# Kernel tuning notes

Measured on AMD Instinct MI355X. Metric: run time of the kernel, lower is better.

The kernel has to match this reference:

```python
import math
import jax, jax.numpy as jnp
import numpy as np

B, T, C, H = 2, 2048, 1024, 16
D = C // H


def get_slopes(n):
    def pow2_slopes(n):
        start = 2.0 ** (-(2.0 ** (-(math.log2(n) - 3))))
        return [start * (start ** i) for i in range(n)]
    if math.log2(n).is_integer():
        return pow2_slopes(n)
    c = 2 ** math.floor(math.log2(n))
    return pow2_slopes(c) + get_slopes(2 * c)[0::2][: n - c]


def setup_inputs() -> dict:
    key = jax.random.key(0)
    ks = jax.random.split(key, 5)
    std = 0.02
    x = jax.random.normal(ks[0], (B, T, C), dtype=jnp.float32)
    Wq = std * jax.random.normal(ks[1], (C, C), dtype=jnp.float32)
    Wk = std * jax.random.normal(ks[2], (C, C), dtype=jnp.float32)
    Wv = std * jax.random.normal(ks[3], (C, C), dtype=jnp.float32)
    Wo = (std / math.sqrt(24)) * jax.random.normal(ks[4], (C, C), dtype=jnp.float32)
    z = jnp.zeros((C,), dtype=jnp.float32)
    return {"x": x, "Wq": Wq, "bq": z, "Wk": Wk, "bk": z, "Wv": Wv, "bv": z, "Wo": Wo, "bo": z}


def reference(x, Wq, bq, Wk, bk, Wv, bv, Wo, bo):
    b, t, c = x.shape
    h, d = H, c // H
    # qkv projections: nn.Linear computes x @ W.T + b
    q = (x @ Wq.T + bq).reshape(b, t, h, d).transpose(0, 2, 1, 3)  # [B,H,T,D]
    k = (x @ Wk.T + bk).reshape(b, t, h, d).transpose(0, 2, 1, 3)
    v = (x @ Wv.T + bv).reshape(b, t, h, d).transpose(0, 2, 1, 3)

    att = jnp.einsum("bhqd,bhkd->bhqk", q, k) * (1.0 / math.sqrt(d))

    # ALiBi bias: -slope_h * (i - j) on the lower triangle, 0 above
    slopes = jnp.asarray(get_slopes(h), dtype=x.dtype)  # [H]
    i = jnp.arange(t)
    rel = jnp.tril(i[:, None] - i[None, :]).astype(x.dtype)  # [T,T]
    alibi = -slopes[:, None, None] * rel  # [H,T,T]
    att = att + alibi[None, :, :, :]

    causal = jnp.tril(jnp.ones((t, t), dtype=bool))
    att = jnp.where(causal[None, None, :, :], att, -jnp.inf)
    att = jax.nn.softmax(att, axis=-1)

    y = jnp.einsum("bhqk,bhkd->bhqd", att, v)
    y = y.transpose(0, 2, 1, 3).reshape(b, t, c)
    return y @ Wo.T + bo
```

## Files before the change

kernel.cpp:

```cpp
#include <hip/hip_runtime.h>
#include <hip/hip_bf16.h>
#include <cstdint>
#include <cstddef>

#define B_ 2
#define T_ 2048
#define C_ 1024
#define H_ 16
#define D_ 64
#define BT_ (B_*T_)
#define QKV_S 3072

typedef __bf16 bf16;
typedef __bf16 bf16x4 __attribute__((ext_vector_type(4)));
typedef __bf16 bf16x8 __attribute__((ext_vector_type(8)));
typedef float f32x4 __attribute__((ext_vector_type(4)));

__global__ __launch_bounds__(256) void cast_f32_bf16(const float* __restrict__ in,
                                                     bf16* __restrict__ out, int n) {
  int stride = gridDim.x * blockDim.x;
  for (int i = blockIdx.x * blockDim.x + threadIdx.x; i * 4 < n; i += stride) {
    float4 v = *reinterpret_cast<const float4*>(in + (size_t)i * 4);
    bf16x4 o;
    o[0] = (bf16)v.x; o[1] = (bf16)v.y; o[2] = (bf16)v.z; o[3] = (bf16)v.w;
    *reinterpret_cast<bf16x4*>(out + (size_t)i * 4) = o;
  }
}

template<typename OutT>
__global__ __launch_bounds__(256) void gemm_bt(const bf16* __restrict__ A,
                                               const bf16* __restrict__ Bm,
                                               const float* __restrict__ bias,
                                               OutT* __restrict__ Cout,
                                               int M, int N, int K) {
  __shared__ bf16 As[128 * 32];
  __shared__ bf16 Bs[128 * 32];
  const int tid = threadIdx.x;
  const int wid = tid >> 6, lane = tid & 63;
  const int grp = lane >> 4, li = lane & 15;
  const int wr = wid >> 1, wc = wid & 1;
  const int m0 = blockIdx.y * 128, n0 = blockIdx.x * 128;

  f32x4 acc[4][4] = {};

  const int srow = lane >> 2;
  const int scol = (lane & 3) * 8;

  for (int k0 = 0; k0 < K; k0 += 32) {
#pragma unroll
    for (int p = 0; p < 2; ++p) {
      const int rbase = (p * 4 + wid) * 16;
      const bf16* ga = A + (size_t)(m0 + rbase + srow) * K + (k0 + scol);
      const bf16* gb = Bm + (size_t)(n0 + rbase + srow) * K + (k0 + scol);
      bf16* la = As + (p * 4 + wid) * 512;
      bf16* lb = Bs + (p * 4 + wid) * 512;
      __builtin_amdgcn_global_load_lds((__attribute__((address_space(1))) void*)ga,
                                       (__attribute__((address_space(3))) void*)la, 16, 0, 0);
      __builtin_amdgcn_global_load_lds((__attribute__((address_space(1))) void*)gb,
                                       (__attribute__((address_space(3))) void*)lb, 16, 0, 0);
    }
    __syncthreads();

    bf16x8 af[4], bfr[4];
#pragma unroll
    for (int m = 0; m < 4; ++m)
      af[m] = *reinterpret_cast<const bf16x8*>(&As[(wr * 64 + m * 16 + li) * 32 + grp * 8]);
#pragma unroll
    for (int n = 0; n < 4; ++n)
      bfr[n] = *reinterpret_cast<const bf16x8*>(&Bs[(wc * 64 + n * 16 + li) * 32 + grp * 8]);
#pragma unroll
    for (int m = 0; m < 4; ++m)
#pragma unroll
      for (int n = 0; n < 4; ++n)
        acc[m][n] = __builtin_amdgcn_mfma_f32_16x16x32_bf16(af[m], bfr[n], acc[m][n], 0, 0, 0);
    __syncthreads();
  }

  float bcol[4];
#pragma unroll
  for (int n = 0; n < 4; ++n) bcol[n] = bias[n0 + wc * 64 + n * 16 + li];
#pragma unroll
  for (int m = 0; m < 4; ++m) {
#pragma unroll
    for (int n = 0; n < 4; ++n) {
      const int col = n0 + wc * 64 + n * 16 + li;
#pragma unroll
      for (int j = 0; j < 4; ++j) {
        const int row = m0 + wr * 64 + m * 16 + grp * 4 + j;
        float v = acc[m][n][j] + bcol[n];
        Cout[(size_t)row * N + col] = (OutT)v;
      }
    }
  }
}

__global__ __launch_bounds__(256) void transpose_v(const bf16* __restrict__ qkv,
                                                   bf16* __restrict__ Vt) {
  __shared__ bf16 tile[64 * 72];
  const int tid = threadIdx.x;
  const int t0 = blockIdx.x * 64, bh = blockIdx.y;
  const int b = bh >> 4, h = bh & 15;
#pragma unroll
  for (int p = 0; p < 2; ++p) {
    int idx = p * 256 + tid;
    int r = idx >> 3, c = (idx & 7) * 8;
    bf16x8 v = *reinterpret_cast<const bf16x8*>(qkv + (size_t)(b * T_ + t0 + r) * QKV_S + 2 * C_ + h * D_ + c);
    *reinterpret_cast<bf16x8*>(&tile[r * 72 + c]) = v;
  }
  __syncthreads();
#pragma unroll
  for (int p = 0; p < 2; ++p) {
    int idx = p * 256 + tid;
    int d = idx >> 3, tc = (idx & 7) * 8;
    bf16x8 o;
#pragma unroll
    for (int j = 0; j < 8; ++j) o[j] = tile[(tc + j) * 72 + d];
    *reinterpret_cast<bf16x8*>(Vt + ((size_t)bh * D_ + d) * T_ + t0 + tc) = o;
  }
}

__global__ __launch_bounds__(256) void attn_kernel(const bf16* __restrict__ qkv,
                                                   const bf16* __restrict__ Vt,
                                                   bf16* __restrict__ Y) {
  __shared__ bf16 Ks[2][64 * 64];
  __shared__ bf16 Vs[2][64 * 64];
  __shared__ bf16 Ps[4 * 16 * 72];

  const int tid = threadIdx.x;
  const int wid = tid >> 6, lane = tid & 63;
  const int grp = lane >> 4, li = lane & 15;
  const int qt = gridDim.x - 1 - blockIdx.x;
  const int bh = blockIdx.y;
  const int b = bh >> 4, h = bh & 15;
  const int q0 = qt * 64;
  const int qi = q0 + wid * 16 + li;
  const float slope = exp2f(-0.5f * (float)(h + 1));

  bf16* Pw = Ps + wid * (16 * 72);

  bf16x8 qf[2];
  {
    const bf16* qrow = qkv + (size_t)(b * T_ + qi) * QKV_S + h * D_;
    qf[0] = *reinterpret_cast<const bf16x8*>(qrow + grp * 8);
    qf[1] = *reinterpret_cast<const bf16x8*>(qrow + 32 + grp * 8);
#pragma unroll
    for (int c = 0; c < 2; ++c)
#pragma unroll
      for (int j = 0; j < 8; ++j)
        qf[c][j] = (bf16)((float)qf[c][j] * 0.125f);
  }

  f32x4 oacc[4] = {};
  float mrun = -1e30f, lrun = 0.f;

  const bf16* Kbase = qkv + (size_t)b * T_ * QKV_S + C_ + (size_t)h * D_;
  const bf16* Vbase = Vt + (size_t)bh * D_ * T_;

  const int srow = lane >> 3;
  const int sswz = ((lane & 7) * 16) ^ (srow << 4);
  const int rsw = (li & 7) << 4;

  auto stage = [&](int kv0, int bufi) __attribute__((always_inline)) {
#pragma unroll
    for (int p = 0; p < 2; ++p) {
      const int rbase = p * 32 + wid * 8;
      const int row = rbase + srow;
      const bf16* gk = Kbase + (size_t)(kv0 + row) * QKV_S + (sswz >> 1);
      const bf16* gv = Vbase + (size_t)row * T_ + kv0 + (sswz >> 1);
      __builtin_amdgcn_global_load_lds((__attribute__((address_space(1))) void*)gk,
                                       (__attribute__((address_space(3))) void*)(&Ks[bufi][rbase * 64]), 16, 0, 0);
      __builtin_amdgcn_global_load_lds((__attribute__((address_space(1))) void*)gv,
                                       (__attribute__((address_space(3))) void*)(&Vs[bufi][rbase * 64]), 16, 0, 0);
    }
  };

  auto compute = [&](int kv0, int bufi, bool masked) __attribute__((always_inline)) {
    const char* Kb = (const char*)&Ks[bufi][0];
    const char* Vb = (const char*)&Vs[bufi][0];

    f32x4 s[4] = {};
#pragma unroll
    for (int n = 0; n < 4; ++n) {
      const char* kr = Kb + (n * 16 + li) * 128;
      bf16x8 kf0 = *reinterpret_cast<const bf16x8*>(kr + ((grp * 16) ^ rsw));
      bf16x8 kf1 = *reinterpret_cast<const bf16x8*>(kr + ((64 + grp * 16) ^ rsw));
      s[n] = __builtin_amdgcn_mfma_f32_16x16x32_bf16(kf0, qf[0], s[n], 0, 0, 0);
      s[n] = __builtin_amdgcn_mfma_f32_16x16x32_bf16(kf1, qf[1], s[n], 0, 0, 0);
    }

    float p[4][4];
    float rm = -1e30f;
#pragma unroll
    for (int n = 0; n < 4; ++n)
#pragma unroll
      for (int j = 0; j < 4; ++j) {
        const int kv = kv0 + n * 16 + grp * 4 + j;
        float sv = fmaf(-slope, (float)(qi - kv), s[n][j]);
        if (masked) sv = (kv <= qi) ? sv : -1e30f;
        p[n][j] = sv;
        rm = fmaxf(rm, sv);
      }
    rm = fmaxf(rm, __shfl_xor(rm, 16, 64));
    rm = fmaxf(rm, __shfl_xor(rm, 32, 64));
    const float mnew = fmaxf(mrun, rm);
    const float alpha = __expf(mrun - mnew);
    mrun = mnew;
    float rs = 0.f;
#pragma unroll
    for (int n = 0; n < 4; ++n)
#pragma unroll
      for (int j = 0; j < 4; ++j) {
        float e = __expf(p[n][j] - mnew);
        p[n][j] = e;
        rs += e;
      }
    rs += __shfl_xor(rs, 16, 64);
    rs += __shfl_xor(rs, 32, 64);
    lrun = lrun * alpha + rs;
#pragma unroll
    for (int nd = 0; nd < 4; ++nd)
#pragma unroll
      for (int j = 0; j < 4; ++j)
        oacc[nd][j] *= alpha;

#pragma unroll
    for (int n = 0; n < 4; ++n) {
      bf16x4 p4;
#pragma unroll
      for (int j = 0; j < 4; ++j) p4[j] = (bf16)p[n][j];
      *reinterpret_cast<bf16x4*>(Pw + li * 72 + n * 16 + grp * 4) = p4;
    }
    asm volatile("s_waitcnt lgkmcnt(0)" ::: "memory");
    __builtin_amdgcn_sched_barrier(0);

#pragma unroll
    for (int kc = 0; kc < 2; ++kc) {
      bf16x8 pb = *reinterpret_cast<const bf16x8*>(Pw + li * 72 + kc * 32 + grp * 8);
#pragma unroll
      for (int nd = 0; nd < 4; ++nd) {
        const char* vrp = Vb + (nd * 16 + li) * 128;
        bf16x8 vf = *reinterpret_cast<const bf16x8*>(vrp + ((kc * 64 + grp * 16) ^ rsw));
        oacc[nd] = __builtin_amdgcn_mfma_f32_16x16x32_bf16(vf, pb, oacc[nd], 0, 0, 0);
      }
    }
  };

  const int nt = qt + 1;
  stage(0, 0);
  __syncthreads();
  int cur = 0;
  for (int t = 0; t < nt; ++t) {
    if (t + 1 < nt) stage((t + 1) * 64, cur ^ 1);
    compute(t * 64, cur, t == nt - 1);
    __syncthreads();
    cur ^= 1;
  }

  const float rinv = 1.f / lrun;
#pragma unroll
  for (int nd = 0; nd < 4; ++nd) {
    bf16x4 o4;
#pragma unroll
    for (int j = 0; j < 4; ++j) o4[j] = (bf16)(oacc[nd][j] * rinv);
    *reinterpret_cast<bf16x4*>(Pw + li * 72 + nd * 16 + grp * 4) = o4;
  }
  asm volatile("s_waitcnt lgkmcnt(0)" ::: "memory");
  __builtin_amdgcn_sched_barrier(0);
  {
    bf16* yrow = Y + (size_t)(b * T_ + qi) * C_ + h * D_;
#pragma unroll
    for (int c = 0; c < 2; ++c) {
      bf16x8 y8 = *reinterpret_cast<const bf16x8*>(Pw + li * 72 + (c * 4 + grp) * 8);
      *reinterpret_cast<bf16x8*>(yrow + (c * 4 + grp) * 8) = y8;
    }
  }
}

extern "C" void kernel_launch(void* const* d_in, const int* in_sizes, int n_in,
                              void* d_out, int out_size, void* d_ws, size_t ws_size,
                              hipStream_t stream) {
  const float* x  = (const float*)d_in[0];
  const float* Wq = (const float*)d_in[1];
  const float* bq = (const float*)d_in[2];
  const float* Wk = (const float*)d_in[3];
  const float* bk = (const float*)d_in[4];
  const float* Wv = (const float*)d_in[5];
  const float* bv = (const float*)d_in[6];
  const float* Wo = (const float*)d_in[7];
  const float* bo = (const float*)d_in[8];
  float* out = (float*)d_out;

  char* ws = (char*)d_ws;
  bf16* xb    = (bf16*)ws; ws += (size_t)BT_ * C_ * 2;
  bf16* wqkvb = (bf16*)ws; ws += (size_t)3 * C_ * C_ * 2;
  bf16* wob   = (bf16*)ws; ws += (size_t)C_ * C_ * 2;
  bf16* qkvb  = (bf16*)ws; ws += (size_t)BT_ * QKV_S * 2;
  bf16* vtb   = (bf16*)ws; ws += (size_t)B_ * H_ * D_ * T_ * 2;
  float* bqkv = (float*)ws; ws += (size_t)3 * C_ * 4;
  bf16* yb    = xb;

  hipMemcpyAsync(bqkv,          bq, C_ * 4, hipMemcpyDeviceToDevice, stream);
  hipMemcpyAsync(bqkv + C_,     bk, C_ * 4, hipMemcpyDeviceToDevice, stream);
  hipMemcpyAsync(bqkv + 2 * C_, bv, C_ * 4, hipMemcpyDeviceToDevice, stream);

  auto cast = [&](const float* src, bf16* dst, int n) {
    int thr = n / 4;
    int blocks = (thr + 255) / 256;
    if (blocks > 4096) blocks = 4096;
    cast_f32_bf16<<<dim3(blocks), dim3(256), 0, stream>>>(src, dst, n);
  };
  cast(x,  xb,  BT_ * C_);
  cast(Wq, wqkvb,               C_ * C_);
  cast(Wk, wqkvb + C_ * C_,     C_ * C_);
  cast(Wv, wqkvb + 2 * C_ * C_, C_ * C_);
  cast(Wo, wob, C_ * C_);

  gemm_bt<bf16><<<dim3(QKV_S / 128, BT_ / 128), dim3(256), 0, stream>>>(xb, wqkvb, bqkv, qkvb, BT_, QKV_S, C_);

  transpose_v<<<dim3(T_ / 64, B_ * H_), dim3(256), 0, stream>>>(qkvb, vtb);

  attn_kernel<<<dim3(T_ / 64, B_ * H_), dim3(256), 0, stream>>>(qkvb, vtb, yb);

  gemm_bt<float><<<dim3(C_ / 128, BT_ / 128), dim3(256), 0, stream>>>(yb, wob, bo, out, BT_, C_, C_);
}
```

Before: 260.2 us.

## Enlarge attention query tile to 128 rows with 8 waves and MFMA priority hints

The attention kernel now handles 128 query rows per block with 512 threads (8 waves), so each staged K/V tile in LDS serves twice as many query rows and each thread issues one async load per tile instead of two. Per-wave causal skipping avoids compute on tiles entirely past a wave's rows, and the diagonal mask is applied per wave. s_setprio raises wave priority around the MFMA sections to favour matrix issue. In exchange, the grid has half as many blocks, which lowers parallelism, and waves in the lower half of a block sit idle at barriers while the upper half finishes the extra tiles.

Result: faster. 243.2 us (-6.5%).

```diff
diff --git a/kernel.cpp b/kernel.cpp
--- a/kernel.cpp
+++ b/kernel.cpp
@@ -119,21 +119,22 @@
   }
 }
 
-__global__ __launch_bounds__(256) void attn_kernel(const bf16* __restrict__ qkv,
+__global__ __launch_bounds__(512) void attn_kernel(const bf16* __restrict__ qkv,
                                                    const bf16* __restrict__ Vt,
                                                    bf16* __restrict__ Y) {
   __shared__ bf16 Ks[2][64 * 64];
   __shared__ bf16 Vs[2][64 * 64];
-  __shared__ bf16 Ps[4 * 16 * 72];
+  __shared__ bf16 Ps[8 * 16 * 72];
 
   const int tid = threadIdx.x;
   const int wid = tid >> 6, lane = tid & 63;
   const int grp = lane >> 4, li = lane & 15;
-  const int qt = gridDim.x - 1 - blockIdx.x;
+  const int QT = gridDim.x - 1 - blockIdx.x;
   const int bh = blockIdx.y;
   const int b = bh >> 4, h = bh & 15;
-  const int q0 = qt * 64;
-  const int qi = q0 + wid * 16 + li;
+  const int q0 = QT * 128;
+  const int wq0 = q0 + wid * 16;
+  const int qi = wq0 + li;
   const float slope = exp2f(-0.5f * (float)(h + 1));
 
   bf16* Pw = Ps + wid * (16 * 72);
@@ -156,22 +157,17 @@
   const bf16* Kbase = qkv + (size_t)b * T_ * QKV_S + C_ + (size_t)h * D_;
   const bf16* Vbase = Vt + (size_t)bh * D_ * T_;
 
-  const int srow = lane >> 3;
-  const int sswz = ((lane & 7) * 16) ^ (srow << 4);
+  const int strow = tid >> 3;
+  const int stswz = ((tid & 7) * 16) ^ ((strow & 7) << 4);
   const int rsw = (li & 7) << 4;
 
   auto stage = [&](int kv0, int bufi) __attribute__((always_inline)) {
-#pragma unroll
-    for (int p = 0; p < 2; ++p) {
-      const int rbase = p * 32 + wid * 8;
-      const int row = rbase + srow;
-      const bf16* gk = Kbase + (size_t)(kv0 + row) * QKV_S + (sswz >> 1);
-      const bf16* gv = Vbase + (size_t)row * T_ + kv0 + (sswz >> 1);
-      __builtin_amdgcn_global_load_lds((__attribute__((address_space(1))) void*)gk,
-                                       (__attribute__((address_space(3))) void*)(&Ks[bufi][rbase * 64]), 16, 0, 0);
-      __builtin_amdgcn_global_load_lds((__attribute__((address_space(1))) void*)gv,
-                                       (__attribute__((address_space(3))) void*)(&Vs[bufi][rbase * 64]), 16, 0, 0);
-    }
+    const bf16* gk = Kbase + (size_t)(kv0 + strow) * QKV_S + (stswz >> 1);
+    const bf16* gv = Vbase + (size_t)strow * T_ + kv0 + (stswz >> 1);
+    __builtin_amdgcn_global_load_lds((__attribute__((address_space(1))) void*)gk,
+                                     (__attribute__((address_space(3))) void*)(&Ks[bufi][wid * 512]), 16, 0, 0);
+    __builtin_amdgcn_global_load_lds((__attribute__((address_space(1))) void*)gv,
+                                     (__attribute__((address_space(3))) void*)(&Vs[bufi][wid * 512]), 16, 0, 0);
   };
 
   auto compute = [&](int kv0, int bufi, bool masked) __attribute__((always_inline)) {
@@ -179,6 +175,7 @@
     const char* Vb = (const char*)&Vs[bufi][0];
 
     f32x4 s[4] = {};
+    __builtin_amdgcn_s_setprio(1);
 #pragma unroll
     for (int n = 0; n < 4; ++n) {
       const char* kr = Kb + (n * 16 + li) * 128;
@@ -187,6 +184,7 @@
       s[n] = __builtin_amdgcn_mfma_f32_16x16x32_bf16(kf0, qf[0], s[n], 0, 0, 0);
       s[n] = __builtin_amdgcn_mfma_f32_16x16x32_bf16(kf1, qf[1], s[n], 0, 0, 0);
     }
+    __builtin_amdgcn_s_setprio(0);
 
     float p[4][4];
     float rm = -1e30f;
@@ -233,6 +231,7 @@
     asm volatile("s_waitcnt lgkmcnt(0)" ::: "memory");
     __builtin_amdgcn_sched_barrier(0);
 
+    __builtin_amdgcn_s_setprio(1);
 #pragma unroll
     for (int kc = 0; kc < 2; ++kc) {
       bf16x8 pb = *reinterpret_cast<const bf16x8*>(Pw + li * 72 + kc * 32 + grp * 8);
@@ -243,15 +242,17 @@
         oacc[nd] = __builtin_amdgcn_mfma_f32_16x16x32_bf16(vf, pb, oacc[nd], 0, 0, 0);
       }
     }
+    __builtin_amdgcn_s_setprio(0);
   };
 
-  const int nt = qt + 1;
+  const int nt = 2 * QT + 2;
   stage(0, 0);
   __syncthreads();
   int cur = 0;
   for (int t = 0; t < nt; ++t) {
+    const int kv0 = t * 64;
     if (t + 1 < nt) stage((t + 1) * 64, cur ^ 1);
-    compute(t * 64, cur, t == nt - 1);
+    if (kv0 <= wq0) compute(kv0, cur, kv0 + 64 > wq0);
     __syncthreads();
     cur ^= 1;
   }
@@ -319,7 +320,7 @@
 
   transpose_v<<<dim3(T_ / 64, B_ * H_), dim3(256), 0, stream>>>(qkvb, vtb);
 
-  attn_kernel<<<dim3(T_ / 64, B_ * H_), dim3(256), 0, stream>>>(qkvb, vtb, yb);
+  attn_kernel<<<dim3(T_ / 128, B_ * H_), dim3(512), 0, stream>>>(qkvb, vtb, yb);
 
   gemm_bt<float><<<dim3(C_ / 128, BT_ / 128), dim3(256), 0, stream>>>(yb, wob, bo, out, BT_, C_, C_);
 }
```
